# Kernel optimization log

Hardware: AMD Instinct MI355X
Metric: run time of the kernel (lower is better)

Reference implementation:

```python
import jax, jax.numpy as jnp
import numpy as np

B, S, D, FF, E = 4, 2048, 1024, 4096, 8


def setup_inputs() -> dict:
    key = jax.random.key(0)
    ks = jax.random.split(key, 6)
    scale_r = 1.0 / np.sqrt(D)
    return {
        "x": jax.random.normal(ks[0], (B, S, D), dtype=jnp.float32),
        "W_router": jax.random.normal(ks[1], (D, E), dtype=jnp.float32) * scale_r,
        "W1": jax.random.normal(ks[2], (E, D, FF), dtype=jnp.float32) * (1.0 / np.sqrt(D)),
        "b1": jnp.zeros((E, FF), dtype=jnp.float32),
        "W2": jax.random.normal(ks[3], (E, FF, D), dtype=jnp.float32) * (1.0 / np.sqrt(FF)),
        "b2": jnp.zeros((E, D), dtype=jnp.float32),
    }


def reference(x, W_router, W1, b1, W2, b2):
    # Router: softmax over experts, top-2, renormalize the 2 gates with softmax
    logits = jnp.einsum("bsd,de->bse", x, W_router)          # [B,S,E]
    probs = jax.nn.softmax(logits, axis=-1)
    top_vals, top_idx = jax.lax.top_k(probs, 2)               # [B,S,2]
    gates2 = jax.nn.softmax(top_vals, axis=-1)                # [B,S,2]

    num_experts = W1.shape[0]
    out = jnp.zeros_like(x)
    # Faithful masked-dense MoE: each expert runs over all tokens (input masked),
    # output scaled by its gate (0 for non-selected tokens).
    for i in range(num_experts):
        sel = (top_idx == i)                                  # [B,S,2] bool
        mask = jnp.any(sel, axis=-1, keepdims=True).astype(x.dtype)  # [B,S,1]
        xi = x * mask
        h = jax.nn.gelu(jnp.einsum("bsd,df->bsf", xi, W1[i]) + b1[i], approximate=False)
        yi = jnp.einsum("bsf,fd->bsd", h, W2[i]) + b2[i]
        g = jnp.sum(gates2 * sel.astype(x.dtype), axis=-1, keepdims=True)  # [B,S,1]
        out = out + yi * g
    return out
```

## Files before the change

kernel.cpp:

```cpp
#include <hip/hip_runtime.h>
#include <hip/hip_bf16.h>
#include <math.h>

#define NEXP 8
#define DDIM 1024
#define FFDIM 4096
#define NTOK 8192
#define NSLOT (NTOK * 2)
#define BM 128
#define BN 128
#define BK 64
#define MAXT ((NSLOT / BM) + NEXP)

typedef __attribute__((ext_vector_type(8))) __bf16 bf16x8;
typedef __attribute__((ext_vector_type(4))) __bf16 bf16x4;
typedef __attribute__((ext_vector_type(4))) float f32x4;

union BF8 { __bf16 b[8]; uint4 u; bf16x8 v; };

__device__ __forceinline__ float gelu_fast(float v) {
    float vv = v * v;
    float ex = __expf(v * fmaf(0.0713548162726f, vv, 1.59576912161f));
    float s = __builtin_amdgcn_rcpf(ex + 1.0f);
    return v * (1.0f - s);
}

__device__ __forceinline__ int swz(int row, int colb) {
    return row * 128 + (colb ^ ((row & 7) << 4));
}

__global__ __launch_bounds__(64)
void router_kernel(const float* __restrict__ x, const float* __restrict__ Wr,
                   int* __restrict__ idx2, float* __restrict__ gates2,
                   int* __restrict__ counts)
{
    int t = blockIdx.x;
    int lane = threadIdx.x;
    const float* xr = x + (size_t)t * DDIM;
    float acc[NEXP];
#pragma unroll
    for (int e = 0; e < NEXP; ++e) acc[e] = 0.f;
    for (int d = lane; d < DDIM; d += 64) {
        float xv = xr[d];
        const float* wrow = Wr + d * NEXP;
#pragma unroll
        for (int e = 0; e < NEXP; ++e) acc[e] += xv * wrow[e];
    }
#pragma unroll
    for (int e = 0; e < NEXP; ++e) {
        float v = acc[e];
        for (int off = 32; off > 0; off >>= 1) v += __shfl_xor(v, off, 64);
        acc[e] = v;
    }
    if (lane == 0) {
        float mx = acc[0];
#pragma unroll
        for (int e = 1; e < NEXP; ++e) mx = fmaxf(mx, acc[e]);
        float p[NEXP]; float s = 0.f;
#pragma unroll
        for (int e = 0; e < NEXP; ++e) { p[e] = expf(acc[e] - mx); s += p[e]; }
        float inv = 1.f / s;
#pragma unroll
        for (int e = 0; e < NEXP; ++e) p[e] *= inv;
        int i1 = 0; float p1 = p[0];
#pragma unroll
        for (int e = 1; e < NEXP; ++e) if (p[e] > p1) { p1 = p[e]; i1 = e; }
        int i2 = -1; float p2 = -1.f;
#pragma unroll
        for (int e = 0; e < NEXP; ++e) {
            if (e == i1) continue;
            if (p[e] > p2) { p2 = p[e]; i2 = e; }
        }
        float u = expf(p2 - p1);
        float den = 1.f + u;
        idx2[2 * t] = i1; idx2[2 * t + 1] = i2;
        gates2[2 * t] = 1.f / den; gates2[2 * t + 1] = u / den;
        atomicAdd(&counts[i1], 1);
        atomicAdd(&counts[i2], 1);
    }
}

__global__ __launch_bounds__(256)
void offsets_kernel(const int* __restrict__ counts, int* __restrict__ offsets,
                    int* __restrict__ cursors, int* __restrict__ tiletab)
{
    __shared__ int soff[NEXP], stile[NEXP + 1];
    int tid = threadIdx.x;
    if (tid == 0) {
        int off = 0, tt = 0;
        for (int e = 0; e < NEXP; ++e) {
            soff[e] = off; stile[e] = tt;
            int c = counts[e];
            off += c; tt += (c + BM - 1) / BM;
        }
        stile[NEXP] = tt;
    }
    __syncthreads();
    if (tid < NEXP) { offsets[tid] = soff[tid]; cursors[tid] = 0; }
    int total = stile[NEXP];
    for (int i = tid; i < MAXT; i += 256) {
        if (i < total) {
            int e = 0;
            while (stile[e + 1] <= i) ++e;
            tiletab[2 * i] = e; tiletab[2 * i + 1] = i - stile[e];
        } else {
            tiletab[2 * i] = -1; tiletab[2 * i + 1] = 0;
        }
    }
}

__global__ __launch_bounds__(256)
void fill_kernel(const int* __restrict__ idx2, const float* __restrict__ gates2,
                 const int* __restrict__ offsets, int* __restrict__ cursors,
                 int* __restrict__ perm, float* __restrict__ gate_slot,
                 int* __restrict__ tslot)
{
    int t = blockIdx.x * 256 + threadIdx.x;
    if (t >= NTOK) return;
#pragma unroll
    for (int s = 0; s < 2; ++s) {
        int e = idx2[2 * t + s];
        int pos = atomicAdd(&cursors[e], 1);
        int slot = offsets[e] + pos;
        perm[slot] = t;
        gate_slot[slot] = gates2[2 * t + s];
        tslot[2 * t + s] = slot;
    }
}

__global__ __launch_bounds__(256)
void convert_x_kernel(const float* __restrict__ x, __bf16* __restrict__ xb)
{
    size_t i = ((size_t)blockIdx.x * 256 + threadIdx.x) * 8;
    float4 a = *(const float4*)(x + i);
    float4 b = *(const float4*)(x + i + 4);
    BF8 pk;
    pk.b[0] = (__bf16)a.x; pk.b[1] = (__bf16)a.y; pk.b[2] = (__bf16)a.z; pk.b[3] = (__bf16)a.w;
    pk.b[4] = (__bf16)b.x; pk.b[5] = (__bf16)b.y; pk.b[6] = (__bf16)b.z; pk.b[7] = (__bf16)b.w;
    *(uint4*)(xb + i) = pk.u;
}

__global__ __launch_bounds__(128)
void convert_w_kernel(const float* __restrict__ W, __bf16* __restrict__ WT, int K, int N)
{
    int ktiles = K >> 6;
    int nt = blockIdx.x / ktiles;
    int kt = blockIdx.x % ktiles;
    int e = blockIdx.y;
    const float* We = W + (size_t)e * K * N;
    int r = threadIdx.x;
    const float* src = We + (size_t)(kt * 64) * N + nt * 128 + r;
    char* dst = (char*)WT + ((((size_t)e * (N >> 7) + nt) * ktiles + kt) << 14) + r * 128;
    float f[64];
#pragma unroll
    for (int j = 0; j < 64; ++j) f[j] = src[(size_t)j * N];
#pragma unroll
    for (int gi = 0; gi < 8; ++gi) {
        BF8 pk;
#pragma unroll
        for (int q = 0; q < 8; ++q) pk.b[q] = (__bf16)f[gi * 8 + q];
        *(uint4*)(dst + ((gi * 16) ^ ((r & 7) << 4))) = pk.u;
    }
}

__device__ __forceinline__ bool tile_header(const int* counts, const int* offsets,
                                            const int* tiletab, int e_arg, int c_arg, int CH,
                                            int tile_idx,
                                            int& e, int& start, int& cnt, int& hbase, int& row0,
                                            int& rows_here)
{
    int rowtile;
    if (e_arg >= 0) {
        e = e_arg;
        int cbase = c_arg * CH;
        cnt = counts[e] - cbase;
        if (cnt <= 0) return false;
        if (cnt > CH) cnt = CH;
        start = offsets[e] + cbase;
        rowtile = tile_idx;
        hbase = start;
    } else {
        e = tiletab[2 * tile_idx];
        if (e < 0) return false;
        rowtile = tiletab[2 * tile_idx + 1];
        start = offsets[e];
        cnt = counts[e];
        hbase = 0;
    }
    row0 = rowtile * BM;
    if (row0 >= cnt) return false;
    rows_here = cnt - row0;
    if (rows_here > BM) rows_here = BM;
    return true;
}

__global__ __launch_bounds__(256)
void gemm1_fast(const __bf16* __restrict__ xb, const __bf16* __restrict__ W1T,
                const float* __restrict__ b1,
                const int* __restrict__ perm, const int* __restrict__ counts,
                const int* __restrict__ offsets, const int* __restrict__ tiletab,
                __bf16* __restrict__ H, int e_arg, int c_arg, int CH)
{
    __shared__ __align__(16) char smem[(BM + BN) * 128];
    char* As = smem;
    char* Bs = smem + BM * 128;

    int e, start, cnt, hbase, row0, rows_here;
    if (!tile_header(counts, offsets, tiletab, e_arg, c_arg, CH, blockIdx.y,
                     e, start, cnt, hbase, row0, rows_here))
        return;

    const float* b1e = b1 + (size_t)e * FFDIM;
    int nt = blockIdx.x;
    int n0 = nt * BN;
    const char* bsrc = (const char*)W1T + ((((size_t)e * (FFDIM >> 7) + nt) * (DDIM >> 6)) << 14);

    int tid = threadIdx.x;
    int lane = tid & 63;
    int wid = tid >> 6;
    int wm = wid >> 1, wn = wid & 1;
    int lr = lane & 15, lhi = lane >> 4;

    int ar = tid >> 1, ach = tid & 1;
    int token = -1;
    if (ar < rows_here) token = perm[start + row0 + ar];
    const __bf16* arow = xb + (size_t)(token < 0 ? 0 : token) * DDIM + ach * 32;

    int boff = wid * 4096 + lane * 16;

    f32x4 acc[4][4] = {};

    for (int kt = 0; kt < DDIM / BK; ++kt) {
        __syncthreads();
        {
            uint4 v[4];
            if (token >= 0) {
                const uint4* p = (const uint4*)(arow + kt * BK);
#pragma unroll
                for (int i = 0; i < 4; ++i) v[i] = p[i];
            } else {
#pragma unroll
                for (int i = 0; i < 4; ++i) v[i] = make_uint4(0u, 0u, 0u, 0u);
            }
#pragma unroll
            for (int i = 0; i < 4; ++i)
                *(uint4*)(As + swz(ar, ach * 64 + i * 16)) = v[i];
        }
        {
            const char* tsrc = bsrc + ((size_t)kt << 14);
#pragma unroll
            for (int j = 0; j < 4; ++j) {
                uint4 v = *(const uint4*)(tsrc + j * 1024 + boff);
                *(uint4*)(Bs + j * 1024 + boff) = v;
            }
        }
        __syncthreads();

#pragma unroll
        for (int kk = 0; kk < 2; ++kk) {
            bf16x8 af[4], bfr[4];
#pragma unroll
            for (int m = 0; m < 4; ++m)
                af[m] = *(const bf16x8*)(As + swz(wm * 64 + m * 16 + lr, kk * 64 + lhi * 16));
#pragma unroll
            for (int n = 0; n < 4; ++n)
                bfr[n] = *(const bf16x8*)(Bs + swz(wn * 64 + n * 16 + lr, kk * 64 + lhi * 16));
#pragma unroll
            for (int m = 0; m < 4; ++m)
#pragma unroll
                for (int n = 0; n < 4; ++n)
                    acc[m][n] = __builtin_amdgcn_mfma_f32_16x16x32_bf16(af[m], bfr[n], acc[m][n], 0, 0, 0);
        }
    }

    float bias[4];
#pragma unroll
    for (int n = 0; n < 4; ++n) bias[n] = b1e[n0 + wn * 64 + n * 16 + lr];

#pragma unroll
    for (int m = 0; m < 4; ++m) {
        int rbase = wm * 64 + m * 16 + lhi * 4;
#pragma unroll
        for (int j = 0; j < 4; ++j) {
            int rl = rbase + j;
            if (rl < rows_here) {
                __bf16* hr = H + (size_t)(start + row0 + rl - hbase) * FFDIM + n0 + wn * 64;
#pragma unroll
                for (int n = 0; n < 4; ++n) {
                    float v = acc[m][n][j] + bias[n];
                    hr[n * 16 + lr] = (__bf16)gelu_fast(v);
                }
            }
        }
    }
}

__global__ __launch_bounds__(256)
void gemm2_fast(const __bf16* __restrict__ H, const __bf16* __restrict__ W2T,
                const float* __restrict__ b2,
                const int* __restrict__ perm, const float* __restrict__ gate_slot,
                const int* __restrict__ counts, const int* __restrict__ offsets,
                const int* __restrict__ tiletab,
                float* __restrict__ out, __bf16* __restrict__ Y, int use_y,
                int e_arg, int c_arg, int CH)
{
    __shared__ __align__(16) char smem[(BM + BN) * 128];
    char* As = smem;
    char* Bs = smem + BM * 128;

    int e, start, cnt, hbase, row0, rows_here;
    if (!tile_header(counts, offsets, tiletab, e_arg, c_arg, CH, blockIdx.y,
                     e, start, cnt, hbase, row0, rows_here))
        return;

    const float* b2e = b2 + (size_t)e * DDIM;
    int nt = blockIdx.x;
    int n0 = nt * BN;
    const char* bsrc = (const char*)W2T + ((((size_t)e * (DDIM >> 7) + nt) * (FFDIM >> 6)) << 14);

    int tid = threadIdx.x;
    int lane = tid & 63;
    int wid = tid >> 6;
    int wm = wid >> 1, wn = wid & 1;
    int lr = lane & 15, lhi = lane >> 4;

    int ar = tid >> 1, ach = tid & 1;
    bool aval = (ar < rows_here);
    const __bf16* hrow = H + (size_t)(aval ? (start + row0 + ar - hbase) : 0) * FFDIM + ach * 32;

    int boff = wid * 4096 + lane * 16;

    f32x4 acc[4][4] = {};

    for (int kt = 0; kt < FFDIM / BK; ++kt) {
        __syncthreads();
        {
            uint4 v[4];
            if (aval) {
                const uint4* p = (const uint4*)(hrow + kt * BK);
#pragma unroll
                for (int i = 0; i < 4; ++i) v[i] = p[i];
            } else {
#pragma unroll
                for (int i = 0; i < 4; ++i) v[i] = make_uint4(0u, 0u, 0u, 0u);
            }
#pragma unroll
            for (int i = 0; i < 4; ++i)
                *(uint4*)(As + swz(ar, ach * 64 + i * 16)) = v[i];
        }
        {
            const char* tsrc = bsrc + ((size_t)kt << 14);
#pragma unroll
            for (int j = 0; j < 4; ++j) {
                uint4 v = *(const uint4*)(tsrc + j * 1024 + boff);
                *(uint4*)(Bs + j * 1024 + boff) = v;
            }
        }
        __syncthreads();

#pragma unroll
        for (int kk = 0; kk < 2; ++kk) {
            bf16x8 af[4], bfr[4];
#pragma unroll
            for (int m = 0; m < 4; ++m)
                af[m] = *(const bf16x8*)(As + swz(wm * 64 + m * 16 + lr, kk * 64 + lhi * 16));
#pragma unroll
            for (int n = 0; n < 4; ++n)
                bfr[n] = *(const bf16x8*)(Bs + swz(wn * 64 + n * 16 + lr, kk * 64 + lhi * 16));
#pragma unroll
            for (int m = 0; m < 4; ++m)
#pragma unroll
                for (int n = 0; n < 4; ++n)
                    acc[m][n] = __builtin_amdgcn_mfma_f32_16x16x32_bf16(af[m], bfr[n], acc[m][n], 0, 0, 0);
        }
    }

    float bias[4];
#pragma unroll
    for (int n = 0; n < 4; ++n) bias[n] = b2e[n0 + wn * 64 + n * 16 + lr];

#pragma unroll
    for (int m = 0; m < 4; ++m) {
        int rbase = wm * 64 + m * 16 + lhi * 4;
#pragma unroll
        for (int j = 0; j < 4; ++j) {
            int rl = rbase + j;
            if (rl < rows_here) {
                int slot = start + row0 + rl;
                float g = gate_slot[slot];
                if (use_y) {
                    __bf16* yrow = Y + (size_t)slot * DDIM + n0 + wn * 64;
#pragma unroll
                    for (int n = 0; n < 4; ++n)
                        yrow[n * 16 + lr] = (__bf16)((acc[m][n][j] + bias[n]) * g);
                } else {
                    int token = perm[slot];
                    float* orow = out + (size_t)token * DDIM + n0 + wn * 64;
#pragma unroll
                    for (int n = 0; n < 4; ++n)
                        atomicAdd(orow + n * 16 + lr, (acc[m][n][j] + bias[n]) * g);
                }
            }
        }
    }
}

__global__ __launch_bounds__(256)
void combine_kernel(const __bf16* __restrict__ Y, const int* __restrict__ tslot,
                    float* __restrict__ out)
{
    int t = blockIdx.x;
    int c = threadIdx.x * 4;
    int sa = tslot[2 * t], sb = tslot[2 * t + 1];
    bf16x4 a = *(const bf16x4*)(Y + (size_t)sa * DDIM + c);
    bf16x4 b = *(const bf16x4*)(Y + (size_t)sb * DDIM + c);
    float4 r;
    r.x = (float)a[0] + (float)b[0];
    r.y = (float)a[1] + (float)b[1];
    r.z = (float)a[2] + (float)b[2];
    r.w = (float)a[3] + (float)b[3];
    *(float4*)(out + (size_t)t * DDIM + c) = r;
}

__global__ __launch_bounds__(256)
void gemm1_legacy(const float* __restrict__ x, const float* __restrict__ W1,
                  const float* __restrict__ b1,
                  const int* __restrict__ perm, const int* __restrict__ counts,
                  const int* __restrict__ offsets, const int* __restrict__ tiletab,
                  __bf16* __restrict__ H, int e_arg, int c_arg, int CH)
{
    __shared__ __align__(16) char smem[(BM + BN) * 128];
    char* As = smem;
    char* Bs = smem + BM * 128;

    int e, start, cnt, hbase, row0, rows_here;
    if (!tile_header(counts, offsets, tiletab, e_arg, c_arg, CH, blockIdx.y,
                     e, start, cnt, hbase, row0, rows_here))
        return;

    const float* W1e = W1 + (size_t)e * DDIM * FFDIM;
    const float* b1e = b1 + (size_t)e * FFDIM;
    int n0 = blockIdx.x * BN;

    int tid = threadIdx.x;
    int lane = tid & 63;
    int wid = tid >> 6;
    int wm = wid >> 1, wn = wid & 1;
    int lr = lane & 15, lhi = lane >> 4;

    int ar = tid >> 1, ach = tid & 1;
    int token = -1;
    if (ar < rows_here) token = perm[start + row0 + ar];
    const float* arow = x + (size_t)(token < 0 ? 0 : token) * DDIM + ach * 32;

    int bn = tid & 127, bkh = tid >> 7;
    const float* bcol = W1e + (size_t)bkh * 32 * FFDIM + n0 + bn;

    f32x4 acc[4][4] = {};

    for (int k0 = 0; k0 < DDIM; k0 += BK) {
        __syncthreads();
        {
            BF8 pk[4];
            if (token >= 0) {
                const float4* p = (const float4*)(arow + k0);
#pragma unroll
                for (int i = 0; i < 4; ++i) {
                    float4 v0 = p[2 * i], v1 = p[2 * i + 1];
                    pk[i].b[0] = (__bf16)v0.x; pk[i].b[1] = (__bf16)v0.y;
                    pk[i].b[2] = (__bf16)v0.z; pk[i].b[3] = (__bf16)v0.w;
                    pk[i].b[4] = (__bf16)v1.x; pk[i].b[5] = (__bf16)v1.y;
                    pk[i].b[6] = (__bf16)v1.z; pk[i].b[7] = (__bf16)v1.w;
                }
            } else {
#pragma unroll
                for (int i = 0; i < 4; ++i) pk[i].u = make_uint4(0u, 0u, 0u, 0u);
            }
#pragma unroll
            for (int i = 0; i < 4; ++i)
                *(uint4*)(As + swz(ar, ach * 64 + i * 16)) = pk[i].u;
        }
        {
            float f[32];
            const float* p = bcol + (size_t)k0 * FFDIM;
#pragma unroll
            for (int j = 0; j < 32; ++j) f[j] = p[(size_t)j * FFDIM];
#pragma unroll
            for (int i = 0; i < 4; ++i) {
                BF8 pk;
#pragma unroll
                for (int q = 0; q < 8; ++q) pk.b[q] = (__bf16)f[i * 8 + q];
                *(uint4*)(Bs + swz(bn, bkh * 64 + i * 16)) = pk.u;
            }
        }
        __syncthreads();

#pragma unroll
        for (int kk = 0; kk < 2; ++kk) {
            bf16x8 af[4], bfr[4];
#pragma unroll
            for (int m = 0; m < 4; ++m)
                af[m] = *(const bf16x8*)(As + swz(wm * 64 + m * 16 + lr, kk * 64 + lhi * 16));
#pragma unroll
            for (int n = 0; n < 4; ++n)
                bfr[n] = *(const bf16x8*)(Bs + swz(wn * 64 + n * 16 + lr, kk * 64 + lhi * 16));
#pragma unroll
            for (int m = 0; m < 4; ++m)
#pragma unroll
                for (int n = 0; n < 4; ++n)
                    acc[m][n] = __builtin_amdgcn_mfma_f32_16x16x32_bf16(af[m], bfr[n], acc[m][n], 0, 0, 0);
        }
    }

    float bias[4];
#pragma unroll
    for (int n = 0; n < 4; ++n) bias[n] = b1e[n0 + wn * 64 + n * 16 + lr];

#pragma unroll
    for (int m = 0; m < 4; ++m) {
        int rbase = wm * 64 + m * 16 + lhi * 4;
#pragma unroll
        for (int j = 0; j < 4; ++j) {
            int rl = rbase + j;
            if (rl < rows_here) {
                __bf16* hr = H + (size_t)(start + row0 + rl - hbase) * FFDIM + n0 + wn * 64;
#pragma unroll
                for (int n = 0; n < 4; ++n) {
                    float v = acc[m][n][j] + bias[n];
                    hr[n * 16 + lr] = (__bf16)gelu_fast(v);
                }
            }
        }
    }
}

__global__ __launch_bounds__(256)
void gemm2_legacy(const __bf16* __restrict__ H, const float* __restrict__ W2,
                  const float* __restrict__ b2,
                  const int* __restrict__ perm, const float* __restrict__ gate_slot,
                  const int* __restrict__ counts, const int* __restrict__ offsets,
                  const int* __restrict__ tiletab,
                  float* __restrict__ out, int e_arg, int c_arg, int CH)
{
    __shared__ __align__(16) char smem[(BM + BN) * 128];
    char* As = smem;
    char* Bs = smem + BM * 128;

    int e, start, cnt, hbase, row0, rows_here;
    if (!tile_header(counts, offsets, tiletab, e_arg, c_arg, CH, blockIdx.y,
                     e, start, cnt, hbase, row0, rows_here))
        return;

    const float* W2e = W2 + (size_t)e * FFDIM * DDIM;
    const float* b2e = b2 + (size_t)e * DDIM;
    int n0 = blockIdx.x * BN;

    int tid = threadIdx.x;
    int lane = tid & 63;
    int wid = tid >> 6;
    int wm = wid >> 1, wn = wid & 1;
    int lr = lane & 15, lhi = lane >> 4;

    int ar = tid >> 1, ach = tid & 1;
    bool aval = (ar < rows_here);
    const __bf16* hrow = H + (size_t)(aval ? (start + row0 + ar - hbase) : 0) * FFDIM + ach * 32;

    int bn = tid & 127, bkh = tid >> 7;
    const float* bcol = W2e + (size_t)bkh * 32 * DDIM + n0 + bn;

    f32x4 acc[4][4] = {};

    for (int k0 = 0; k0 < FFDIM; k0 += BK) {
        __syncthreads();
        {
            uint4 v[4];
            if (aval) {
                const uint4* p = (const uint4*)(hrow + k0);
#pragma unroll
                for (int i = 0; i < 4; ++i) v[i] = p[i];
            } else {
#pragma unroll
                for (int i = 0; i < 4; ++i) v[i] = make_uint4(0u, 0u, 0u, 0u);
            }
#pragma unroll
            for (int i = 0; i < 4; ++i)
                *(uint4*)(As + swz(ar, ach * 64 + i * 16)) = v[i];
        }
        {
            float f[32];
            const float* p = bcol + (size_t)k0 * DDIM;
#pragma unroll
            for (int j = 0; j < 32; ++j) f[j] = p[(size_t)j * DDIM];
#pragma unroll
            for (int i = 0; i < 4; ++i) {
                BF8 pk;
#pragma unroll
                for (int q = 0; q < 8; ++q) pk.b[q] = (__bf16)f[i * 8 + q];
                *(uint4*)(Bs + swz(bn, bkh * 64 + i * 16)) = pk.u;
            }
        }
        __syncthreads();

#pragma unroll
        for (int kk = 0; kk < 2; ++kk) {
            bf16x8 af[4], bfr[4];
#pragma unroll
            for (int m = 0; m < 4; ++m)
                af[m] = *(const bf16x8*)(As + swz(wm * 64 + m * 16 + lr, kk * 64 + lhi * 16));
#pragma unroll
            for (int n = 0; n < 4; ++n)
                bfr[n] = *(const bf16x8*)(Bs + swz(wn * 64 + n * 16 + lr, kk * 64 + lhi * 16));
#pragma unroll
            for (int m = 0; m < 4; ++m)
#pragma unroll
                for (int n = 0; n < 4; ++n)
                    acc[m][n] = __builtin_amdgcn_mfma_f32_16x16x32_bf16(af[m], bfr[n], acc[m][n], 0, 0, 0);
        }
    }

    float bias[4];
#pragma unroll
    for (int n = 0; n < 4; ++n) bias[n] = b2e[n0 + wn * 64 + n * 16 + lr];

#pragma unroll
    for (int m = 0; m < 4; ++m) {
        int rbase = wm * 64 + m * 16 + lhi * 4;
#pragma unroll
        for (int j = 0; j < 4; ++j) {
            int rl = rbase + j;
            if (rl < rows_here) {
                int slot = start + row0 + rl;
                int token = perm[slot];
                float g = gate_slot[slot];
                float* orow = out + (size_t)token * DDIM + n0 + wn * 64;
#pragma unroll
                for (int n = 0; n < 4; ++n) {
                    float v = (acc[m][n][j] + bias[n]) * g;
                    atomicAdd(orow + n * 16 + lr, v);
                }
            }
        }
    }
}

extern "C" void kernel_launch(void* const* d_in, const int* in_sizes, int n_in,
                              void* d_out, int out_size, void* d_ws, size_t ws_size,
                              hipStream_t stream)
{
    const float* x  = (const float*)d_in[0];
    const float* Wr = (const float*)d_in[1];
    const float* W1 = (const float*)d_in[2];
    const float* b1 = (const float*)d_in[3];
    const float* W2 = (const float*)d_in[4];
    const float* b2 = (const float*)d_in[5];
    float* out = (float*)d_out;

    char* ws = (char*)d_ws;
    int* counts   = (int*)ws;
    int* offsets  = counts + 8;
    int* cursors  = offsets + 8;
    int* tiletab  = cursors + 8;
    int* idx2     = tiletab + 2 * MAXT;
    float* gates2 = (float*)(idx2 + 2 * NTOK);
    int* perm     = (int*)(gates2 + 2 * NTOK);
    float* gate_slot = (float*)(perm + NSLOT);
    int* tslot    = (int*)(gate_slot + NSLOT);
    char* hraw = (char*)(tslot + 2 * NTOK);
    size_t small_end = (((size_t)(hraw - ws)) + 255) & ~(size_t)255;

    __bf16* xb  = (__bf16*)(ws + small_end);
    __bf16* W1T = xb + (size_t)NTOK * DDIM;
    __bf16* W2T = W1T + (size_t)NEXP * DDIM * FFDIM;
    __bf16* Hf  = W2T + (size_t)NEXP * FFDIM * DDIM;
    __bf16* Y   = W1T;
    size_t fast_off = small_end + ((size_t)NTOK * DDIM + 2 * (size_t)NEXP * DDIM * FFDIM) * 2;
    size_t availHf = ws_size > fast_off ? ws_size - fast_off : 0;
    size_t need_H = (size_t)NSLOT * FFDIM * 2;
    bool have_w = availHf >= (size_t)BM * FFDIM * 2 * 8;

    hipMemsetAsync(counts, 0, 8 * sizeof(int), stream);

    router_kernel<<<NTOK, 64, 0, stream>>>(x, Wr, idx2, gates2, counts);
    if (have_w) {
        convert_x_kernel<<<NTOK * DDIM / 2048, 256, 0, stream>>>(x, xb);
        convert_w_kernel<<<dim3((FFDIM / 128) * (DDIM / 64), NEXP), 128, 0, stream>>>(W1, W1T, DDIM, FFDIM);
        convert_w_kernel<<<dim3((DDIM / 128) * (FFDIM / 64), NEXP), 128, 0, stream>>>(W2, W2T, FFDIM, DDIM);
    }
    offsets_kernel<<<1, 256, 0, stream>>>(counts, offsets, cursors, tiletab);
    fill_kernel<<<NTOK / 256, 256, 0, stream>>>(idx2, gates2, offsets, cursors, perm, gate_slot, tslot);

    if (have_w && availHf >= need_H) {
        dim3 g1(FFDIM / BN, MAXT, 1);
        gemm1_fast<<<g1, 256, 0, stream>>>(xb, W1T, b1, perm, counts, offsets, tiletab, Hf, -1, 0, 0);
        dim3 g2(DDIM / BN, MAXT, 1);
        gemm2_fast<<<g2, 256, 0, stream>>>(Hf, W2T, b2, perm, gate_slot, counts, offsets, tiletab,
                                           out, Y, 1, -1, 0, 0);
        combine_kernel<<<NTOK, 256, 0, stream>>>(Y, tslot, out);
    } else if (have_w) {
        hipMemsetAsync(d_out, 0, (size_t)out_size * sizeof(float), stream);
        long long chl = (long long)((availHf / ((size_t)FFDIM * 2)) / BM) * BM;
        int CH = (int)(chl > 4096 ? 4096 : chl);
        int nchunk = (NSLOT + CH - 1) / CH;
        for (int e = 0; e < NEXP; ++e) {
            for (int c = 0; c < nchunk; ++c) {
                dim3 g1(FFDIM / BN, CH / BM, 1);
                gemm1_fast<<<g1, 256, 0, stream>>>(xb, W1T, b1, perm, counts, offsets, tiletab, Hf, e, c, CH);
                dim3 g2(DDIM / BN, CH / BM, 1);
                gemm2_fast<<<g2, 256, 0, stream>>>(Hf, W2T, b2, perm, gate_slot, counts, offsets, tiletab,
                                                   out, (__bf16*)nullptr, 0, e, c, CH);
            }
        }
    } else {
        hipMemsetAsync(d_out, 0, (size_t)out_size * sizeof(float), stream);
        __bf16* H = (__bf16*)(ws + small_end);
        size_t avail = ws_size > small_end ? ws_size - small_end : 0;
        if (avail >= need_H) {
            dim3 g1(FFDIM / BN, MAXT, 1);
            gemm1_legacy<<<g1, 256, 0, stream>>>(x, W1, b1, perm, counts, offsets, tiletab, H, -1, 0, 0);
            dim3 g2(DDIM / BN, MAXT, 1);
            gemm2_legacy<<<g2, 256, 0, stream>>>(H, W2, b2, perm, gate_slot, counts, offsets, tiletab, out, -1, 0, 0);
        } else {
            long long chl = (long long)((avail / ((size_t)FFDIM * 2)) / BM) * BM;
            int CH = (int)(chl > 2048 ? 2048 : chl);
            if (CH >= BM) {
                int nchunk = (NSLOT + CH - 1) / CH;
                for (int e = 0; e < NEXP; ++e) {
                    for (int c = 0; c < nchunk; ++c) {
                        dim3 g1(FFDIM / BN, CH / BM, 1);
                        gemm1_legacy<<<g1, 256, 0, stream>>>(x, W1, b1, perm, counts, offsets, tiletab, H, e, c, CH);
                        dim3 g2(DDIM / BN, CH / BM, 1);
                        gemm2_legacy<<<g2, 256, 0, stream>>>(H, W2, b2, perm, gate_slot, counts, offsets, tiletab, out, e, c, CH);
                    }
                }
            }
        }
    }
}
```

Before: 807.2 us.

## Load weight tiles directly into LDS and remap blocks across XCDs

The B (weight) tiles in both expert GEMMs are now fetched with global_load_lds, which writes straight into shared memory instead of going through registers. Launches become 1D, and block indices are remapped so consecutive logical tiles land on the same XCD, aiming for better L2 reuse of weights and activations. This lowers register and VGPR traffic for the B tiles. The risk is that the async LDS writes must be fully complete before the barrier, and the remap changes the tile scheduling order.

New measurement: 805.3 us. No clear change (-0.2%).

```diff
diff --git a/kernel.cpp b/kernel.cpp
--- a/kernel.cpp
+++ b/kernel.cpp
@@ -18,6 +18,12 @@
 
 union BF8 { __bf16 b[8]; uint4 u; bf16x8 v; };
 
+typedef const __attribute__((address_space(1))) void* gptr1_t;
+typedef __attribute__((address_space(3))) void* lptr3_t;
+__device__ __forceinline__ void gll16(const void* g, void* l) {
+    __builtin_amdgcn_global_load_lds((gptr1_t)g, (lptr3_t)l, 16, 0, 0);
+}
+
 __device__ __forceinline__ float gelu_fast(float v) {
     float vv = v * v;
     float ex = __expf(v * fmaf(0.0713548162726f, vv, 1.59576912161f));
@@ -27,6 +33,11 @@
 
 __device__ __forceinline__ int swz(int row, int colb) {
     return row * 128 + (colb ^ ((row & 7) << 4));
+}
+
+__device__ __forceinline__ int xcd_logical(int bid, int nwg) {
+    if (nwg & 7) return bid;
+    return (bid & 7) * (nwg >> 3) + (bid >> 3);
 }
 
 __global__ __launch_bounds__(64)
@@ -205,13 +216,21 @@
     char* As = smem;
     char* Bs = smem + BM * 128;
 
+    const int NTN = FFDIM / BN;
+    int tile_idx, nt;
+    if (e_arg >= 0) { nt = blockIdx.x; tile_idx = blockIdx.y; }
+    else {
+        int L = xcd_logical(blockIdx.x, gridDim.x);
+        nt = L % NTN;
+        tile_idx = L / NTN;
+    }
+
     int e, start, cnt, hbase, row0, rows_here;
-    if (!tile_header(counts, offsets, tiletab, e_arg, c_arg, CH, blockIdx.y,
+    if (!tile_header(counts, offsets, tiletab, e_arg, c_arg, CH, tile_idx,
                      e, start, cnt, hbase, row0, rows_here))
         return;
 
     const float* b1e = b1 + (size_t)e * FFDIM;
-    int nt = blockIdx.x;
     int n0 = nt * BN;
     const char* bsrc = (const char*)W1T + ((((size_t)e * (FFDIM >> 7) + nt) * (DDIM >> 6)) << 14);
 
@@ -226,12 +245,16 @@
     if (ar < rows_here) token = perm[start + row0 + ar];
     const __bf16* arow = xb + (size_t)(token < 0 ? 0 : token) * DDIM + ach * 32;
 
-    int boff = wid * 4096 + lane * 16;
+    const char* bwave = bsrc + wid * 4096 + lane * 16;
+    char* bldsb = Bs + wid * 4096;
 
     f32x4 acc[4][4] = {};
 
     for (int kt = 0; kt < DDIM / BK; ++kt) {
         __syncthreads();
+#pragma unroll
+        for (int j = 0; j < 4; ++j)
+            gll16(bwave + ((size_t)kt << 14) + j * 1024, bldsb + j * 1024);
         {
             uint4 v[4];
             if (token >= 0) {
@@ -245,14 +268,6 @@
 #pragma unroll
             for (int i = 0; i < 4; ++i)
                 *(uint4*)(As + swz(ar, ach * 64 + i * 16)) = v[i];
-        }
-        {
-            const char* tsrc = bsrc + ((size_t)kt << 14);
-#pragma unroll
-            for (int j = 0; j < 4; ++j) {
-                uint4 v = *(const uint4*)(tsrc + j * 1024 + boff);
-                *(uint4*)(Bs + j * 1024 + boff) = v;
-            }
         }
         __syncthreads();
 
@@ -308,13 +323,21 @@
     char* As = smem;
     char* Bs = smem + BM * 128;
 
+    const int NTN = DDIM / BN;
+    int tile_idx, nt;
+    if (e_arg >= 0) { nt = blockIdx.x; tile_idx = blockIdx.y; }
+    else {
+        int L = xcd_logical(blockIdx.x, gridDim.x);
+        nt = L % NTN;
+        tile_idx = L / NTN;
+    }
+
     int e, start, cnt, hbase, row0, rows_here;
-    if (!tile_header(counts, offsets, tiletab, e_arg, c_arg, CH, blockIdx.y,
+    if (!tile_header(counts, offsets, tiletab, e_arg, c_arg, CH, tile_idx,
                      e, start, cnt, hbase, row0, rows_here))
         return;
 
     const float* b2e = b2 + (size_t)e * DDIM;
-    int nt = blockIdx.x;
     int n0 = nt * BN;
     const char* bsrc = (const char*)W2T + ((((size_t)e * (DDIM >> 7) + nt) * (FFDIM >> 6)) << 14);
 
@@ -328,12 +351,16 @@
     bool aval = (ar < rows_here);
     const __bf16* hrow = H + (size_t)(aval ? (start + row0 + ar - hbase) : 0) * FFDIM + ach * 32;
 
-    int boff = wid * 4096 + lane * 16;
+    const char* bwave = bsrc + wid * 4096 + lane * 16;
+    char* bldsb = Bs + wid * 4096;
 
     f32x4 acc[4][4] = {};
 
     for (int kt = 0; kt < FFDIM / BK; ++kt) {
         __syncthreads();
+#pragma unroll
+        for (int j = 0; j < 4; ++j)
+            gll16(bwave + ((size_t)kt << 14) + j * 1024, bldsb + j * 1024);
         {
             uint4 v[4];
             if (aval) {
@@ -347,14 +374,6 @@
 #pragma unroll
             for (int i = 0; i < 4; ++i)
                 *(uint4*)(As + swz(ar, ach * 64 + i * 16)) = v[i];
-        }
-        {
-            const char* tsrc = bsrc + ((size_t)kt << 14);
-#pragma unroll
-            for (int j = 0; j < 4; ++j) {
-                uint4 v = *(const uint4*)(tsrc + j * 1024 + boff);
-                *(uint4*)(Bs + j * 1024 + boff) = v;
-            }
         }
         __syncthreads();
 
@@ -690,11 +709,10 @@
     fill_kernel<<<NTOK / 256, 256, 0, stream>>>(idx2, gates2, offsets, cursors, perm, gate_slot, tslot);
 
     if (have_w && availHf >= need_H) {
-        dim3 g1(FFDIM / BN, MAXT, 1);
-        gemm1_fast<<<g1, 256, 0, stream>>>(xb, W1T, b1, perm, counts, offsets, tiletab, Hf, -1, 0, 0);
-        dim3 g2(DDIM / BN, MAXT, 1);
-        gemm2_fast<<<g2, 256, 0, stream>>>(Hf, W2T, b2, perm, gate_slot, counts, offsets, tiletab,
-                                           out, Y, 1, -1, 0, 0);
+        gemm1_fast<<<(FFDIM / BN) * MAXT, 256, 0, stream>>>(xb, W1T, b1, perm, counts, offsets,
+                                                            tiletab, Hf, -1, 0, 0);
+        gemm2_fast<<<(DDIM / BN) * MAXT, 256, 0, stream>>>(Hf, W2T, b2, perm, gate_slot, counts,
+                                                           offsets, tiletab, out, Y, 1, -1, 0, 0);
         combine_kernel<<<NTOK, 256, 0, stream>>>(Y, tslot, out);
     } else if (have_w) {
         hipMemsetAsync(d_out, 0, (size_t)out_size * sizeof(float), stream);
```
